# Performance work log

Measured on AMD Instinct MI355X. Metric: run time of the kernel, lower is better.

## Reference

```python
import jax, jax.numpy as jnp
import numpy as np

SURROGATE_BETA = 10.0

@jax.custom_jvp
def spike_fn(x):
    return jnp.heaviside(x, 1.0)

@spike_fn.defjvp
def _spike_fn_jvp(primals, tangents):
    (x,) = primals
    (x_dot,) = tangents
    return spike_fn(x), x_dot / (1.0 + SURROGATE_BETA * jnp.abs(x))


def setup_inputs() -> dict:
    key = jax.random.key(0)
    k1, k2 = jax.random.split(key)
    B, T, H = 64, 1000, 512
    x = jax.random.normal(k1, (B, T, H), dtype=jnp.float32)
    # learnable decay constants (alpha, beta), will be clamped to [0.5, 1.0]
    decay_constants = jnp.array([0.95, 0.9], dtype=jnp.float32)
    threshold = jnp.array(1.0, dtype=jnp.float32)
    return {"x": x, "decay_constants": decay_constants, "threshold": threshold}


def reference(x, decay_constants, threshold):
    # x: (B, T, H). LIF recurrence over time, vectorized over (B, H).
    alpha = jax.lax.clamp(0.5, decay_constants[0], 1.0)  # membrane decay
    beta = jax.lax.clamp(0.5, decay_constants[1], 1.0)   # synaptic decay
    B, T, H = x.shape
    x_tbh = jnp.swapaxes(x, 0, 1)  # (T, B, H) for scan over time

    def step(carry, x_t):
        mem_pot, syn_curr, spike_out = carry
        # reset_val is None -> reset_pot = mem_pot * spike_out
        reset_pot = jax.lax.stop_gradient(mem_pot * spike_out)  # stop_reset_grad=True
        mem_pot = mem_pot - reset_pot
        mem_pot = alpha * mem_pot + (1.0 - alpha) * syn_curr
        syn_curr = beta * syn_curr + (1.0 - beta) * x_t
        spike_out = spike_fn(mem_pot - threshold)
        return (mem_pot, syn_curr, spike_out), spike_out

    zeros = jnp.zeros((B, H), dtype=jnp.float32)
    init = (zeros, zeros, zeros)
    _, spikes = jax.lax.scan(step, init, x_tbh)  # spikes: (T, B, H)
    return jnp.swapaxes(spikes, 0, 1)  # (B, T, H)
```

## Files before the change

### kernel.cpp

```cpp
#include <hip/hip_runtime.h>


#define LIF_B 64
#define LIF_T 1000
#define LIF_H 512
#define LIF_U 20

__global__ __launch_bounds__(64) void lif_kernel(
    const float* __restrict__ x,
    const float* __restrict__ decay,
    const float* __restrict__ thr_p,
    float* __restrict__ out)
{
    const int n = blockIdx.x * 64 + threadIdx.x;
    const int b = n >> 9;
    const int h = n & (LIF_H - 1);

    const float alpha = fminf(fmaxf(decay[0], 0.5f), 1.0f);
    const float beta  = fminf(fmaxf(decay[1], 0.5f), 1.0f);
    const float oma = __fsub_rn(1.0f, alpha);
    const float omb = __fsub_rn(1.0f, beta);
    const float thr = thr_p[0];

    const size_t base = (size_t)b * LIF_T * LIF_H + h;
    const float* xp = x + base;
    float* op = out + base;

    float mem = 0.0f, syn = 0.0f, spike = 0.0f;

#define LIF_STEP(xv, tt) do {                                              \
        const float reset_ = __fmul_rn(mem, spike);                        \
        mem = __fsub_rn(mem, reset_);                                      \
        mem = __fadd_rn(__fmul_rn(alpha, mem), __fmul_rn(oma, syn));       \
        syn = __fadd_rn(__fmul_rn(beta, syn), __fmul_rn(omb, (xv)));       \
        spike = (__fsub_rn(mem, thr) >= 0.0f) ? 1.0f : 0.0f;               \
        __builtin_nontemporal_store(spike, &op[(size_t)(tt) * LIF_H]);     \
    } while (0)

    float bufA[LIF_U], bufB[LIF_U];
    #pragma unroll
    for (int u = 0; u < LIF_U; ++u) bufA[u] = xp[(size_t)u * LIF_H];
    #pragma unroll
    for (int u = 0; u < LIF_U; ++u) bufB[u] = xp[(size_t)(LIF_U + u) * LIF_H];

    for (int t = 0; t < LIF_T - 2 * LIF_U; t += 2 * LIF_U) {
        #pragma unroll
        for (int u = 0; u < LIF_U; ++u) LIF_STEP(bufA[u], t + u);
        #pragma unroll
        for (int u = 0; u < LIF_U; ++u)
            bufA[u] = xp[(size_t)(t + 2 * LIF_U + u) * LIF_H];

        #pragma unroll
        for (int u = 0; u < LIF_U; ++u) LIF_STEP(bufB[u], t + LIF_U + u);
        #pragma unroll
        for (int u = 0; u < LIF_U; ++u)
            bufB[u] = xp[(size_t)(t + 3 * LIF_U + u) * LIF_H];
    }

    #pragma unroll
    for (int u = 0; u < LIF_U; ++u) LIF_STEP(bufA[u], (LIF_T - 2 * LIF_U) + u);
    #pragma unroll
    for (int u = 0; u < LIF_U; ++u) LIF_STEP(bufB[u], (LIF_T - LIF_U) + u);

#undef LIF_STEP
}

extern "C" void kernel_launch(void* const* d_in, const int* in_sizes, int n_in,
                              void* d_out, int out_size, void* d_ws, size_t ws_size,
                              hipStream_t stream) {
    const float* x     = (const float*)d_in[0];
    const float* decay = (const float*)d_in[1];
    const float* thr   = (const float*)d_in[2];
    float* out = (float*)d_out;

    const int total = LIF_B * LIF_H;
    const int block = 64;
    const int grid  = total / block;
    lif_kernel<<<grid, block, 0, stream>>>(x, decay, thr, out);
}
```

Baseline: 245.9 us.

## Process two neurons per thread with float2 I/O and triple-buffered prefetch

Each thread now runs two independent LIF recurrences on adjacent hidden units, loading and storing float2 vectors, and the grid is halved. The input prefetch moves from double to triple buffering so loads for two chunks ahead are issued before computing the current one. This aims to raise instruction-level and memory-level parallelism per wave in a latency-bound scan, at the cost of fewer waves in total and higher register use.

```diff
diff --git a/kernel.cpp b/kernel.cpp
--- a/kernel.cpp
+++ b/kernel.cpp
@@ -5,16 +5,19 @@
 #define LIF_T 1000
 #define LIF_H 512
 #define LIF_U 20
+#define LIF_W (LIF_H / 2)
 
-__global__ __launch_bounds__(64) void lif_kernel(
+typedef float f2 __attribute__((ext_vector_type(2)));
+
+__global__ __launch_bounds__(64, 1) void lif_kernel(
     const float* __restrict__ x,
     const float* __restrict__ decay,
     const float* __restrict__ thr_p,
     float* __restrict__ out)
 {
-    const int n = blockIdx.x * 64 + threadIdx.x;
-    const int b = n >> 9;
-    const int h = n & (LIF_H - 1);
+    const int n  = blockIdx.x * 64 + threadIdx.x;
+    const int b  = n >> 8;
+    const int hp = n & (LIF_W - 1);
 
     const float alpha = fminf(fmaxf(decay[0], 0.5f), 1.0f);
     const float beta  = fminf(fmaxf(decay[1], 0.5f), 1.0f);
@@ -22,45 +25,58 @@
     const float omb = __fsub_rn(1.0f, beta);
     const float thr = thr_p[0];
 
-    const size_t base = (size_t)b * LIF_T * LIF_H + h;
-    const float* xp = x + base;
-    float* op = out + base;
+    const f2* xp = (const f2*)(x + (size_t)b * LIF_T * LIF_H) + hp;
+    f2*       op = (f2*)(out + (size_t)b * LIF_T * LIF_H) + hp;
 
-    float mem = 0.0f, syn = 0.0f, spike = 0.0f;
+    float mem0 = 0.f, syn0 = 0.f, spk0 = 0.f;
+    float mem1 = 0.f, syn1 = 0.f, spk1 = 0.f;
 
-#define LIF_STEP(xv, tt) do {                                              \
-        const float reset_ = __fmul_rn(mem, spike);                        \
-        mem = __fsub_rn(mem, reset_);                                      \
-        mem = __fadd_rn(__fmul_rn(alpha, mem), __fmul_rn(oma, syn));       \
-        syn = __fadd_rn(__fmul_rn(beta, syn), __fmul_rn(omb, (xv)));       \
-        spike = (__fsub_rn(mem, thr) >= 0.0f) ? 1.0f : 0.0f;               \
-        __builtin_nontemporal_store(spike, &op[(size_t)(tt) * LIF_H]);     \
+#define LIF_STEP(v, tt) do {                                               \
+        const float r0_ = __fmul_rn(mem0, spk0);                           \
+        mem0 = __fsub_rn(mem0, r0_);                                       \
+        mem0 = __fadd_rn(__fmul_rn(alpha, mem0), __fmul_rn(oma, syn0));    \
+        syn0 = __fadd_rn(__fmul_rn(beta, syn0), __fmul_rn(omb, (v).x));    \
+        spk0 = (__fsub_rn(mem0, thr) >= 0.0f) ? 1.0f : 0.0f;               \
+        const float r1_ = __fmul_rn(mem1, spk1);                           \
+        mem1 = __fsub_rn(mem1, r1_);                                       \
+        mem1 = __fadd_rn(__fmul_rn(alpha, mem1), __fmul_rn(oma, syn1));    \
+        syn1 = __fadd_rn(__fmul_rn(beta, syn1), __fmul_rn(omb, (v).y));    \
+        spk1 = (__fsub_rn(mem1, thr) >= 0.0f) ? 1.0f : 0.0f;               \
+        f2 s_; s_.x = spk0; s_.y = spk1;                                   \
+        __builtin_nontemporal_store(s_, &op[(size_t)(tt) * LIF_W]);        \
     } while (0)
 
-    float bufA[LIF_U], bufB[LIF_U];
+    f2 B0[LIF_U], B1[LIF_U], B2[LIF_U];
+
     #pragma unroll
-    for (int u = 0; u < LIF_U; ++u) bufA[u] = xp[(size_t)u * LIF_H];
+    for (int u = 0; u < LIF_U; ++u) B0[u] = xp[(size_t)(0 * LIF_U + u) * LIF_W];
     #pragma unroll
-    for (int u = 0; u < LIF_U; ++u) bufB[u] = xp[(size_t)(LIF_U + u) * LIF_H];
+    for (int u = 0; u < LIF_U; ++u) B1[u] = xp[(size_t)(1 * LIF_U + u) * LIF_W];
 
-    for (int t = 0; t < LIF_T - 2 * LIF_U; t += 2 * LIF_U) {
-        #pragma unroll
-        for (int u = 0; u < LIF_U; ++u) LIF_STEP(bufA[u], t + u);
+    for (int c = 0; c < 48; c += 3) {
         #pragma unroll
         for (int u = 0; u < LIF_U; ++u)
-            bufA[u] = xp[(size_t)(t + 2 * LIF_U + u) * LIF_H];
+            B2[u] = xp[(size_t)((c + 2) * LIF_U + u) * LIF_W];
+        #pragma unroll
+        for (int u = 0; u < LIF_U; ++u) LIF_STEP(B0[u], c * LIF_U + u);
 
         #pragma unroll
-        for (int u = 0; u < LIF_U; ++u) LIF_STEP(bufB[u], t + LIF_U + u);
+        for (int u = 0; u < LIF_U; ++u)
+            B0[u] = xp[(size_t)((c + 3) * LIF_U + u) * LIF_W];
+        #pragma unroll
+        for (int u = 0; u < LIF_U; ++u) LIF_STEP(B1[u], (c + 1) * LIF_U + u);
+
         #pragma unroll
         for (int u = 0; u < LIF_U; ++u)
-            bufB[u] = xp[(size_t)(t + 3 * LIF_U + u) * LIF_H];
+            B1[u] = xp[(size_t)((c + 4) * LIF_U + u) * LIF_W];
+        #pragma unroll
+        for (int u = 0; u < LIF_U; ++u) LIF_STEP(B2[u], (c + 2) * LIF_U + u);
     }
 
     #pragma unroll
-    for (int u = 0; u < LIF_U; ++u) LIF_STEP(bufA[u], (LIF_T - 2 * LIF_U) + u);
+    for (int u = 0; u < LIF_U; ++u) LIF_STEP(B0[u], 48 * LIF_U + u);
     #pragma unroll
-    for (int u = 0; u < LIF_U; ++u) LIF_STEP(bufB[u], (LIF_T - LIF_U) + u);
+    for (int u = 0; u < LIF_U; ++u) LIF_STEP(B1[u], 49 * LIF_U + u);
 
 #undef LIF_STEP
 }
@@ -73,7 +89,7 @@
     const float* thr   = (const float*)d_in[2];
     float* out = (float*)d_out;
 
-    const int total = LIF_B * LIF_H;
+    const int total = LIF_B * LIF_H / 2;
     const int block = 64;
     const int grid  = total / block;
     lif_kernel<<<grid, block, 0, stream>>>(x, decay, thr, out);
```

After: 238.8 us. -2.9%, faster.
